# Performance work log

Hardware: AMD Instinct MI355X
Metric: run time of the kernel (lower is better)

Reference implementation:

```python
import jax, jax.numpy as jnp
import numpy as np

B, S, D = 1, 4096, 512
H, DK, DV = 8, 64, 64


def setup_inputs() -> dict:
    key = jax.random.key(0)
    ks = jax.random.split(key, 8)
    s = 1.0 / np.sqrt(D)
    return {
        "queries": jax.random.normal(ks[0], (B, S, D), jnp.float32),
        "keys": jax.random.normal(ks[1], (B, S, D), jnp.float32),
        "values": jax.random.normal(ks[2], (B, S, D), jnp.float32),
        # Linear weights stored as [in, out] for x @ W
        "Wq": jax.random.normal(ks[3], (D, H * DK), jnp.float32) * s,
        "Wk": jax.random.normal(ks[4], (D, H * DK), jnp.float32) * s,
        "Wv": jax.random.normal(ks[5], (D, H * DV), jnp.float32) * s,
        "Wo": jax.random.normal(ks[6], (H * DV, D), jnp.float32) * s,
        "bo": jax.random.normal(ks[7], (D,), jnp.float32) * 0.02,
    }


def reference(queries, keys, values, Wq, Wk, Wv, Wo, bo):
    b, qlen = values.shape[0], queries.shape[1]
    q = (queries @ Wq).reshape(b, qlen, H, DK)
    k = (keys @ Wk).reshape(b, keys.shape[1], H, DK)
    v = (values @ Wv).reshape(b, values.shape[1], H, DV)
    scale = DK ** 0.5
    # naive full attention: materialize [b, h, sq, sk] scores
    scores = jnp.einsum("bqhd,bkhd->bhqk", q, k) / scale
    attn = jax.nn.softmax(scores, axis=-1)
    out = jnp.einsum("bhqk,bkhd->bqhd", attn, v).reshape(b, qlen, H * DV)
    out = out @ Wo + bo          # first fc_out
    out = out @ Wo + bo          # second fc_out (module applies it twice when not reversible)
    return out
```

## Files before the change

### kernel.cpp

```cpp
#include <hip/hip_runtime.h>

#define S_LEN  4096
#define DMODEL 512
#define NH     8
#define HD     64

typedef _Float16 f16x8 __attribute__((ext_vector_type(8)));
typedef _Float16 f16x4 __attribute__((ext_vector_type(4)));
typedef float    f32x4 __attribute__((ext_vector_type(4)));

static __device__ __forceinline__ unsigned short f2h(float x) {
  return __builtin_bit_cast(unsigned short, (_Float16)x);
}

__global__ __launch_bounds__(256) void wtrans_kernel(
    const float* __restrict__ w0, const float* __restrict__ w1,
    const float* __restrict__ w2, const float* __restrict__ w3,
    unsigned short* __restrict__ o0, unsigned short* __restrict__ o1,
    unsigned short* __restrict__ o2, unsigned short* __restrict__ o3)
{
  __shared__ unsigned short T[64 * 72];
  const float* W; unsigned short* O;
  switch (blockIdx.z) {
    case 0:  W = w0; O = o0; break;
    case 1:  W = w1; O = o1; break;
    case 2:  W = w2; O = o2; break;
    default: W = w3; O = o3; break;
  }
  const int tid = threadIdx.x;
  const int k0 = blockIdx.x * 64, n0 = blockIdx.y * 64;
  const int c4 = (tid & 15) * 4;
#pragma unroll
  for (int rp = 0; rp < 4; ++rp) {
    int r = rp * 16 + (tid >> 4);
    float4 x = *(const float4*)(W + (k0 + r) * DMODEL + n0 + c4);
    T[(c4 + 0) * 72 + r] = f2h(x.x);
    T[(c4 + 1) * 72 + r] = f2h(x.y);
    T[(c4 + 2) * 72 + r] = f2h(x.z);
    T[(c4 + 3) * 72 + r] = f2h(x.w);
  }
  __syncthreads();
#pragma unroll
  for (int it = 0; it < 2; ++it) {
    int i = tid + it * 256;
    int nl = i >> 3, c = i & 7;
    *(f16x8*)&O[(n0 + nl) * DMODEL + k0 + c * 8] = *(const f16x8*)&T[nl * 72 + c * 8];
  }
}

__global__ __launch_bounds__(256) void gemm_kernel(
    const void* __restrict__ A0, const void* __restrict__ A1, const void* __restrict__ A2,
    const unsigned short* __restrict__ B0, const unsigned short* __restrict__ B1,
    const unsigned short* __restrict__ B2,
    void* __restrict__ C0, void* __restrict__ C1, void* __restrict__ C2,
    const float* __restrict__ bias, int a_fp32, int c_fp32)
{
  constexpr int K = DMODEL, N = DMODEL;
  __shared__ unsigned short As[64 * 32];
  __shared__ unsigned short Bs[64 * 32];
  const void* Av; const unsigned short* Bt; void* Cv;
  switch (blockIdx.z) {
    case 0:  Av = A0; Bt = B0; Cv = C0; break;
    case 1:  Av = A1; Bt = B1; Cv = C1; break;
    default: Av = A2; Bt = B2; Cv = C2; break;
  }
  const int tid  = threadIdx.x;
  const int lane = tid & 63;
  const int wid  = tid >> 6;
  const int quad = lane >> 4, l16 = lane & 15;
  const int m0 = blockIdx.x * 64, n0 = blockIdx.y * 64;
  const int wm = (wid >> 1) * 32, wn = (wid & 1) * 32;
  const int r  = tid >> 2, ck = (tid & 3) * 8;
  f32x4 acc[2][2] = {};

  for (int k0 = 0; k0 < K; k0 += 32) {
    __syncthreads();
    if (a_fp32) {
      const float* p = (const float*)Av + (m0 + r) * K + k0 + ck;
      float4 x = *(const float4*)p;
      float4 y = *(const float4*)(p + 4);
      f16x8 av;
      av[0] = (_Float16)x.x; av[1] = (_Float16)x.y;
      av[2] = (_Float16)x.z; av[3] = (_Float16)x.w;
      av[4] = (_Float16)y.x; av[5] = (_Float16)y.y;
      av[6] = (_Float16)y.z; av[7] = (_Float16)y.w;
      *(f16x8*)&As[r * 32 + ck] = av;
    } else {
      *(f16x8*)&As[r * 32 + ck] =
          *(const f16x8*)((const unsigned short*)Av + (m0 + r) * K + k0 + ck);
    }
    *(f16x8*)&Bs[r * 32 + ck] = *(const f16x8*)(Bt + (n0 + r) * K + k0 + ck);
    __syncthreads();

    f16x8 a0 = *(const f16x8*)&As[(wm + l16) * 32 + quad * 8];
    f16x8 a1 = *(const f16x8*)&As[(wm + 16 + l16) * 32 + quad * 8];
    f16x8 b0 = *(const f16x8*)&Bs[(wn + l16) * 32 + quad * 8];
    f16x8 b1 = *(const f16x8*)&Bs[(wn + 16 + l16) * 32 + quad * 8];
    acc[0][0] = __builtin_amdgcn_mfma_f32_16x16x32_f16(a0, b0, acc[0][0], 0, 0, 0);
    acc[0][1] = __builtin_amdgcn_mfma_f32_16x16x32_f16(a0, b1, acc[0][1], 0, 0, 0);
    acc[1][0] = __builtin_amdgcn_mfma_f32_16x16x32_f16(a1, b0, acc[1][0], 0, 0, 0);
    acc[1][1] = __builtin_amdgcn_mfma_f32_16x16x32_f16(a1, b1, acc[1][1], 0, 0, 0);
  }

#pragma unroll
  for (int mt = 0; mt < 2; ++mt)
#pragma unroll
    for (int nt = 0; nt < 2; ++nt) {
      int col = n0 + wn + nt * 16 + l16;
      float bv = bias ? bias[col] : 0.f;
#pragma unroll
      for (int g = 0; g < 4; ++g) {
        int row = m0 + wm + mt * 16 + quad * 4 + g;
        float val = acc[mt][nt][g] + bv;
        if (c_fp32) ((float*)Cv)[row * N + col] = val;
        else        ((unsigned short*)Cv)[row * N + col] = f2h(val);
      }
    }
}

__global__ __launch_bounds__(512) void attn_kernel(
    const unsigned short* __restrict__ Qb, const unsigned short* __restrict__ Kb,
    const unsigned short* __restrict__ Vb, unsigned short* __restrict__ Ob)
{
  __shared__ unsigned short Ks[2][64 * 64];
  __shared__ unsigned short Vs[2][64 * 72];
  __shared__ _Float16 Osc[4][64][16];
  __shared__ float    Msc[4][16];
  __shared__ float    Lsc[4][16];

  const int tid  = threadIdx.x;
  const int lane = tid & 63;
  const int wid  = tid >> 6;
  const int qsub = wid & 3;
  const int kh   = wid >> 2;
  const int quad = lane >> 4, l16 = lane & 15;
  const int qb = blockIdx.x, h = blockIdx.y;
  const int hc = h * HD;

  const int qrow = qb * 64 + qsub * 16 + l16;
  const f16x8 bq0 = *(const f16x8*)(Qb + qrow * DMODEL + hc + quad * 8);
  const f16x8 bq1 = *(const f16x8*)(Qb + qrow * DMODEL + hc + 32 + quad * 8);

  f32x4 o[4] = {};
  float m_run = -1e30f, l_run = 0.f;

  for (int kbi = 0; kbi < 32; ++kbi) {
    __syncthreads();
#pragma unroll
    for (int it = 0; it < 2; ++it) {
      int s = it * 512 + tid;
      int khs = s >> 9, n = (s >> 3) & 63, c = s & 7;
      int key = khs * 2048 + kbi * 64 + n;
      *(f16x8*)&Ks[khs][n * 64 + c * 8] =
          *(const f16x8*)(Kb + key * DMODEL + hc + c * 8);
      *(f16x8*)&Vs[khs][n * 72 + c * 8] =
          *(const f16x8*)(Vb + key * DMODEL + hc + c * 8);
    }
    __syncthreads();

    f32x4 sT[4];
#pragma unroll
    for (int kt = 0; kt < 4; ++kt) {
      f32x4 a = {};
      f16x8 ak0 = *(const f16x8*)&Ks[kh][(kt * 16 + l16) * 64 + quad * 8];
      f16x8 ak1 = *(const f16x8*)&Ks[kh][(kt * 16 + l16) * 64 + 32 + quad * 8];
      a = __builtin_amdgcn_mfma_f32_16x16x32_f16(ak0, bq0, a, 0, 0, 0);
      a = __builtin_amdgcn_mfma_f32_16x16x32_f16(ak1, bq1, a, 0, 0, 0);
      sT[kt] = a;
    }

    float vmax = -1e30f;
#pragma unroll
    for (int kt = 0; kt < 4; ++kt)
#pragma unroll
      for (int g = 0; g < 4; ++g) vmax = fmaxf(vmax, sT[kt][g]);
    vmax = fmaxf(vmax, __shfl_xor(vmax, 16));
    vmax = fmaxf(vmax, __shfl_xor(vmax, 32));
    const float mn = fmaxf(m_run, vmax);
    const float alpha = __expf((m_run - mn) * 0.125f);
    m_run = mn;

    float rs = 0.f;
    f16x4 pa[4];
#pragma unroll
    for (int kt = 0; kt < 4; ++kt)
#pragma unroll
      for (int g = 0; g < 4; ++g) {
        float p = __expf((sT[kt][g] - mn) * 0.125f);
        rs += p;
        pa[kt][g] = (_Float16)p;
      }
    rs += __shfl_xor(rs, 16);
    rs += __shfl_xor(rs, 32);
    l_run = l_run * alpha + rs;

    float ag[4];
#pragma unroll
    for (int g = 0; g < 4; ++g) ag[g] = __shfl(alpha, quad * 4 + g);
#pragma unroll
    for (int nt = 0; nt < 4; ++nt)
#pragma unroll
      for (int g = 0; g < 4; ++g) o[nt][g] *= ag[g];

#pragma unroll
    for (int nt = 0; nt < 4; ++nt)
#pragma unroll
      for (int kt = 0; kt < 4; ++kt) {
        f16x4 bv;
#pragma unroll
        for (int j = 0; j < 4; ++j)
          bv[j] = __builtin_bit_cast(_Float16,
                    Vs[kh][(kt * 16 + quad * 4 + j) * 72 + nt * 16 + l16]);
        o[nt] = __builtin_amdgcn_mfma_f32_16x16x16f16(pa[kt], bv, o[nt], 0, 0, 0);
      }
  }

  __syncthreads();
  if (kh == 1) {
    if (quad == 0) { Msc[qsub][l16] = m_run; Lsc[qsub][l16] = l_run; }
#pragma unroll
    for (int nt = 0; nt < 4; ++nt)
#pragma unroll
      for (int g = 0; g < 4; ++g)
        Osc[qsub][lane][nt * 4 + g] = (_Float16)o[nt][g];
  }
  __syncthreads();
  if (kh == 0) {
    const float m1 = Msc[qsub][l16];
    const float l1 = Lsc[qsub][l16];
    const float m  = fmaxf(m_run, m1);
    const float a0 = __expf((m_run - m) * 0.125f);
    const float a1 = __expf((m1 - m) * 0.125f);
    const float rl = 1.f / (l_run * a0 + l1 * a1);
    float a0g[4], a1g[4], rlg[4];
#pragma unroll
    for (int g = 0; g < 4; ++g) {
      a0g[g] = __shfl(a0, quad * 4 + g);
      a1g[g] = __shfl(a1, quad * 4 + g);
      rlg[g] = __shfl(rl, quad * 4 + g);
    }
#pragma unroll
    for (int g = 0; g < 4; ++g) {
      int row = qb * 64 + qsub * 16 + quad * 4 + g;
#pragma unroll
      for (int nt = 0; nt < 4; ++nt) {
        float om = o[nt][g] * a0g[g] + (float)Osc[qsub][lane][nt * 4 + g] * a1g[g];
        Ob[row * DMODEL + hc + nt * 16 + l16] = f2h(om * rlg[g]);
      }
    }
  }
}

extern "C" void kernel_launch(void* const* d_in, const int* in_sizes, int n_in,
                              void* d_out, int out_size, void* d_ws, size_t ws_size,
                              hipStream_t stream) {
  const float* q  = (const float*)d_in[0];
  const float* k  = (const float*)d_in[1];
  const float* v  = (const float*)d_in[2];
  const float* Wq = (const float*)d_in[3];
  const float* Wk = (const float*)d_in[4];
  const float* Wv = (const float*)d_in[5];
  const float* Wo = (const float*)d_in[6];
  const float* bo = (const float*)d_in[7];

  unsigned short* ws  = (unsigned short*)d_ws;
  unsigned short* Wqt = ws;
  unsigned short* Wkt = Wqt + 262144;
  unsigned short* Wvt = Wkt + 262144;
  unsigned short* Wot = Wvt + 262144;
  unsigned short* Qb  = Wot + 262144;
  unsigned short* Kb  = Qb + 2097152;
  unsigned short* Vb  = Kb + 2097152;
  unsigned short* Ab  = Vb + 2097152;
  unsigned short* O1  = Kb;

  wtrans_kernel<<<dim3(8, 8, 4), 256, 0, stream>>>(Wq, Wk, Wv, Wo, Wqt, Wkt, Wvt, Wot);

  gemm_kernel<<<dim3(64, 8, 3), 256, 0, stream>>>(
      q, k, v, Wqt, Wkt, Wvt, Qb, Kb, Vb, nullptr, 1, 0);

  attn_kernel<<<dim3(64, 8), 512, 0, stream>>>(Qb, Kb, Vb, Ab);

  gemm_kernel<<<dim3(64, 8, 1), 256, 0, stream>>>(
      Ab, Ab, Ab, Wot, Wot, Wot, O1, O1, O1, bo, 0, 0);
  gemm_kernel<<<dim3(64, 8, 1), 256, 0, stream>>>(
      O1, O1, O1, Wot, Wot, Wot, d_out, d_out, d_out, bo, 0, 1);
}
```

Before: 229.7 us.

## Fold double output projection into one GEMM and pre-transpose V globally

Folds the two back-to-back Wo projections algebraically into a single GEMM with a precomputed Wo·Wo product and combined bias bo·Wo+bo. The product is computed as an extra slice of the batched projection GEMM, and a tiny kernel computes the bias. V is written transposed to global memory from the projection GEMM epilogue, so the attention kernel loads it as contiguous rows and reads MFMA B-operands as vectors instead of scalar gathers. K shared tiles are also padded to avoid bank conflicts. The risks are strided scalar stores in the transposed-V epilogue and extra fp16 rounding of the fused weight.

New measurement: 214.4 us. 6.7% less time.

```diff
diff --git a/kernel.cpp b/kernel.cpp
--- a/kernel.cpp
+++ b/kernel.cpp
@@ -17,7 +17,8 @@
     const float* __restrict__ w0, const float* __restrict__ w1,
     const float* __restrict__ w2, const float* __restrict__ w3,
     unsigned short* __restrict__ o0, unsigned short* __restrict__ o1,
-    unsigned short* __restrict__ o2, unsigned short* __restrict__ o3)
+    unsigned short* __restrict__ o2, unsigned short* __restrict__ o3,
+    unsigned short* __restrict__ o3s)
 {
   __shared__ unsigned short T[64 * 72];
   const float* W; unsigned short* O;
@@ -38,6 +39,12 @@
     T[(c4 + 1) * 72 + r] = f2h(x.y);
     T[(c4 + 2) * 72 + r] = f2h(x.z);
     T[(c4 + 3) * 72 + r] = f2h(x.w);
+    if (blockIdx.z == 3) {
+      f16x4 st;
+      st[0] = (_Float16)x.x; st[1] = (_Float16)x.y;
+      st[2] = (_Float16)x.z; st[3] = (_Float16)x.w;
+      *(f16x4*)&o3s[(k0 + r) * DMODEL + n0 + c4] = st;
+    }
   }
   __syncthreads();
 #pragma unroll
@@ -48,22 +55,41 @@
   }
 }
 
+__global__ __launch_bounds__(64) void bo2_kernel(
+    const float* __restrict__ Wo, const float* __restrict__ bo,
+    float* __restrict__ bo2)
+{
+  int col = blockIdx.x * 64 + threadIdx.x;
+  float s = bo[col];
+#pragma unroll 8
+  for (int j = 0; j < DMODEL; ++j) s = fmaf(bo[j], Wo[j * DMODEL + col], s);
+  bo2[col] = s;
+}
+
 __global__ __launch_bounds__(256) void gemm_kernel(
-    const void* __restrict__ A0, const void* __restrict__ A1, const void* __restrict__ A2,
+    const void* __restrict__ A0, const void* __restrict__ A1,
+    const void* __restrict__ A2, const void* __restrict__ A3,
     const unsigned short* __restrict__ B0, const unsigned short* __restrict__ B1,
-    const unsigned short* __restrict__ B2,
-    void* __restrict__ C0, void* __restrict__ C1, void* __restrict__ C2,
-    const float* __restrict__ bias, int a_fp32, int c_fp32)
+    const unsigned short* __restrict__ B2, const unsigned short* __restrict__ B3,
+    void* __restrict__ C0, void* __restrict__ C1,
+    void* __restrict__ C2, void* __restrict__ C3,
+    const float* __restrict__ bias, unsigned short* __restrict__ vtg,
+    int a_fp32_mask, int c_fp32_mask)
 {
   constexpr int K = DMODEL, N = DMODEL;
   __shared__ unsigned short As[64 * 32];
   __shared__ unsigned short Bs[64 * 32];
+  const int z = blockIdx.z;
+  if (z == 3 && blockIdx.x >= 8) return;
   const void* Av; const unsigned short* Bt; void* Cv;
-  switch (blockIdx.z) {
+  switch (z) {
     case 0:  Av = A0; Bt = B0; Cv = C0; break;
     case 1:  Av = A1; Bt = B1; Cv = C1; break;
-    default: Av = A2; Bt = B2; Cv = C2; break;
-  }
+    case 2:  Av = A2; Bt = B2; Cv = C2; break;
+    default: Av = A3; Bt = B3; Cv = C3; break;
+  }
+  const int a_fp32 = (a_fp32_mask >> z) & 1;
+  const int c_fp32 = (c_fp32_mask >> z) & 1;
   const int tid  = threadIdx.x;
   const int lane = tid & 63;
   const int wid  = tid >> 6;
@@ -102,6 +128,7 @@
     acc[1][1] = __builtin_amdgcn_mfma_f32_16x16x32_f16(a1, b1, acc[1][1], 0, 0, 0);
   }
 
+  const int do_vt = (vtg != nullptr) && (z == 2);
 #pragma unroll
   for (int mt = 0; mt < 2; ++mt)
 #pragma unroll
@@ -112,18 +139,19 @@
       for (int g = 0; g < 4; ++g) {
         int row = m0 + wm + mt * 16 + quad * 4 + g;
         float val = acc[mt][nt][g] + bv;
-        if (c_fp32) ((float*)Cv)[row * N + col] = val;
-        else        ((unsigned short*)Cv)[row * N + col] = f2h(val);
+        if (do_vt)        vtg[col * S_LEN + row] = f2h(val);
+        else if (c_fp32)  ((float*)Cv)[row * N + col] = val;
+        else              ((unsigned short*)Cv)[row * N + col] = f2h(val);
       }
     }
 }
 
 __global__ __launch_bounds__(512) void attn_kernel(
     const unsigned short* __restrict__ Qb, const unsigned short* __restrict__ Kb,
-    const unsigned short* __restrict__ Vb, unsigned short* __restrict__ Ob)
+    const unsigned short* __restrict__ VtG, unsigned short* __restrict__ Ob)
 {
-  __shared__ unsigned short Ks[2][64 * 64];
-  __shared__ unsigned short Vs[2][64 * 72];
+  __shared__ unsigned short Ks[2][64 * 72];
+  __shared__ unsigned short Vt[2][64 * 72];
   __shared__ _Float16 Osc[4][64][16];
   __shared__ float    Msc[4][16];
   __shared__ float    Lsc[4][16];
@@ -151,10 +179,10 @@
       int s = it * 512 + tid;
       int khs = s >> 9, n = (s >> 3) & 63, c = s & 7;
       int key = khs * 2048 + kbi * 64 + n;
-      *(f16x8*)&Ks[khs][n * 64 + c * 8] =
+      *(f16x8*)&Ks[khs][n * 72 + c * 8] =
           *(const f16x8*)(Kb + key * DMODEL + hc + c * 8);
-      *(f16x8*)&Vs[khs][n * 72 + c * 8] =
-          *(const f16x8*)(Vb + key * DMODEL + hc + c * 8);
+      *(f16x8*)&Vt[khs][n * 72 + c * 8] =
+          *(const f16x8*)(VtG + (hc + n) * S_LEN + khs * 2048 + kbi * 64 + c * 8);
     }
     __syncthreads();
 
@@ -162,8 +190,8 @@
 #pragma unroll
     for (int kt = 0; kt < 4; ++kt) {
       f32x4 a = {};
-      f16x8 ak0 = *(const f16x8*)&Ks[kh][(kt * 16 + l16) * 64 + quad * 8];
-      f16x8 ak1 = *(const f16x8*)&Ks[kh][(kt * 16 + l16) * 64 + 32 + quad * 8];
+      f16x8 ak0 = *(const f16x8*)&Ks[kh][(kt * 16 + l16) * 72 + quad * 8];
+      f16x8 ak1 = *(const f16x8*)&Ks[kh][(kt * 16 + l16) * 72 + 32 + quad * 8];
       a = __builtin_amdgcn_mfma_f32_16x16x32_f16(ak0, bq0, a, 0, 0, 0);
       a = __builtin_amdgcn_mfma_f32_16x16x32_f16(ak1, bq1, a, 0, 0, 0);
       sT[kt] = a;
@@ -206,11 +234,7 @@
     for (int nt = 0; nt < 4; ++nt)
 #pragma unroll
       for (int kt = 0; kt < 4; ++kt) {
-        f16x4 bv;
-#pragma unroll
-        for (int j = 0; j < 4; ++j)
-          bv[j] = __builtin_bit_cast(_Float16,
-                    Vs[kh][(kt * 16 + quad * 4 + j) * 72 + nt * 16 + l16]);
+        f16x4 bv = *(const f16x4*)&Vt[kh][(nt * 16 + l16) * 72 + kt * 16 + quad * 4];
         o[nt] = __builtin_amdgcn_mfma_f32_16x16x16f16(pa[kt], bv, o[nt], 0, 0, 0);
       }
   }
@@ -263,26 +287,31 @@
   const float* Wo = (const float*)d_in[6];
   const float* bo = (const float*)d_in[7];
 
-  unsigned short* ws  = (unsigned short*)d_ws;
-  unsigned short* Wqt = ws;
-  unsigned short* Wkt = Wqt + 262144;
-  unsigned short* Wvt = Wkt + 262144;
-  unsigned short* Wot = Wvt + 262144;
-  unsigned short* Qb  = Wot + 262144;
-  unsigned short* Kb  = Qb + 2097152;
-  unsigned short* Vb  = Kb + 2097152;
-  unsigned short* Ab  = Vb + 2097152;
-  unsigned short* O1  = Kb;
-
-  wtrans_kernel<<<dim3(8, 8, 4), 256, 0, stream>>>(Wq, Wk, Wv, Wo, Wqt, Wkt, Wvt, Wot);
-
-  gemm_kernel<<<dim3(64, 8, 3), 256, 0, stream>>>(
-      q, k, v, Wqt, Wkt, Wvt, Qb, Kb, Vb, nullptr, 1, 0);
-
-  attn_kernel<<<dim3(64, 8), 512, 0, stream>>>(Qb, Kb, Vb, Ab);
+  unsigned short* ws   = (unsigned short*)d_ws;
+  unsigned short* Wqt  = ws;
+  unsigned short* Wkt  = Wqt  + 262144;
+  unsigned short* Wvt  = Wkt  + 262144;
+  unsigned short* Wot  = Wvt  + 262144;
+  unsigned short* Wof  = Wot  + 262144;
+  unsigned short* Wo2t = Wof  + 262144;
+  unsigned short* Qb   = Wo2t + 262144;
+  unsigned short* Kb   = Qb   + 2097152;
+  unsigned short* VtG  = Kb   + 2097152;
+  unsigned short* Ab   = VtG  + 2097152;
+  float*          bo2  = (float*)(Ab + 2097152);
+
+  wtrans_kernel<<<dim3(8, 8, 4), 256, 0, stream>>>(
+      Wq, Wk, Wv, Wo, Wqt, Wkt, Wvt, Wot, Wof);
+
+  bo2_kernel<<<dim3(8), 64, 0, stream>>>(Wo, bo, bo2);
+
+  gemm_kernel<<<dim3(64, 8, 4), 256, 0, stream>>>(
+      q, k, v, Wot, Wqt, Wkt, Wvt, Wof, Qb, Kb, nullptr, Wo2t,
+      nullptr, VtG, 0x7, 0x0);
+
+  attn_kernel<<<dim3(64, 8), 512, 0, stream>>>(Qb, Kb, VtG, Ab);
 
   gemm_kernel<<<dim3(64, 8, 1), 256, 0, stream>>>(
-      Ab, Ab, Ab, Wot, Wot, Wot, O1, O1, O1, bo, 0, 0);
-  gemm_kernel<<<dim3(64, 8, 1), 256, 0, stream>>>(
-      O1, O1, O1, Wot, Wot, Wot, d_out, d_out, d_out, bo, 0, 1);
-}
+      Ab, nullptr, nullptr, nullptr, Wo2t, nullptr, nullptr, nullptr,
+      d_out, nullptr, nullptr, nullptr, bo2, nullptr, 0x0, 0x1);
+}
```
